# Kernel tuning notes

Hardware: AMD Instinct MI355X
Metric: run time of the kernel (lower is better)

The kernel has to match this reference:

```python
import jax, jax.numpy as jnp
import numpy as np

N = 100000        # num nodes
E = 3_200_000     # num edges
NFEAT, NHID, NCLASS = 256, 128, 40
BN_EPS = 1e-5


def _gcn_norm(edge_index, edge_weight, num_nodes):
    """PyG gcn_norm with self-loops (fill value 1.0): returns (src, dst, norm)."""
    loop = jnp.arange(num_nodes)
    src = jnp.concatenate([edge_index[0], loop])
    dst = jnp.concatenate([edge_index[1], loop])
    ew = jnp.concatenate([edge_weight, jnp.ones((num_nodes,), edge_weight.dtype)])
    deg = jax.ops.segment_sum(ew, dst, num_segments=num_nodes)
    dinv = jnp.where(deg > 0, jax.lax.rsqrt(jnp.maximum(deg, 1e-30)), 0.0)
    norm = dinv[src] * ew * dinv[dst]  # [E+N]
    return src, dst, norm


def _gcn_layer(h, W, b, src, dst, norm, num_nodes):
    lin = h @ W                                   # [N, out]
    msg = lin[src] * norm[:, None]                # gather + scale  [E+N, out]
    agg = jax.ops.segment_sum(msg, dst, num_segments=num_nodes)
    return agg + b


def _bn(h, gamma, beta):
    # BatchNorm1d in training mode: biased batch statistics
    m = jnp.mean(h, axis=0)
    v = jnp.mean(jnp.square(h - m), axis=0)
    return (h - m) * jax.lax.rsqrt(v + BN_EPS) * gamma + beta


def setup_inputs() -> dict:
    key = jax.random.key(0)
    ks = jax.random.split(key, 12)
    s_in = 1.0 / np.sqrt(NFEAT)
    s_h = 1.0 / np.sqrt(NHID)
    return {
        "x": jax.random.normal(ks[0], (N, NFEAT), jnp.float32),
        "edge_index": jax.random.randint(ks[1], (2, E), 0, N, dtype=jnp.int32),
        "edge_weight": jax.random.uniform(ks[2], (E,), jnp.float32),
        "W1": jax.random.normal(ks[3], (NFEAT, NHID), jnp.float32) * s_in,
        "b1": jnp.zeros((NHID,), jnp.float32),
        "g1": jnp.ones((NHID,), jnp.float32),
        "beta1": jnp.zeros((NHID,), jnp.float32),
        "W2": jax.random.normal(ks[4], (NHID, NHID), jnp.float32) * s_h,
        "b2": jnp.zeros((NHID,), jnp.float32),
        "g2": jnp.ones((NHID,), jnp.float32),
        "beta2": jnp.zeros((NHID,), jnp.float32),
        "W3": jax.random.normal(ks[5], (NHID, NHID), jnp.float32) * s_h,
        "b3": jnp.zeros((NHID,), jnp.float32),
        "g3": jnp.ones((NHID,), jnp.float32),
        "beta3": jnp.zeros((NHID,), jnp.float32),
        "linW": jax.random.normal(ks[6], (3 * NHID, NCLASS), jnp.float32) / np.sqrt(3 * NHID),
        "linb": jnp.zeros((NCLASS,), jnp.float32),
    }


def reference(x, edge_index, edge_weight,
              W1, b1, g1, beta1,
              W2, b2, g2, beta2,
              W3, b3, g3, beta3,
              linW, linb):
    src, dst, norm = _gcn_norm(edge_index, edge_weight, N)
    x1 = _bn(jax.nn.relu(_gcn_layer(x, W1, b1, src, dst, norm, N)), g1, beta1)
    x2 = _bn(jax.nn.relu(_gcn_layer(x1, W2, b2, src, dst, norm, N)), g2, beta2)
    x3 = _bn(_gcn_layer(x2, W3, b3, src, dst, norm, N), g3, beta3)  # note: no relu on x3
    embed_x = jnp.concatenate([x1, x2, x3], axis=1)  # [N, 3*NHID]
    logits = embed_x @ linW + linb                   # [N, NCLASS]
    return logits, jax.nn.softmax(logits, axis=1), embed_x
```

## Files before the change

### kernel.cpp

```cpp
#include <hip/hip_runtime.h>
#include <hip/hip_bf16.h>
#include <hip/hip_fp16.h>
#include <math.h>

#define NN 100000
#define NE 3200000
#define NF 256
#define NH 128
#define NC 40
#define BN_EPS 1e-5f

typedef __attribute__((ext_vector_type(8))) short bf16x8;
typedef __attribute__((ext_vector_type(4))) float f32x4;

__device__ __forceinline__ float2 bf2_unpack(unsigned int v) {
    return make_float2(__uint_as_float(v << 16), __uint_as_float(v & 0xffff0000u));
}
__device__ __forceinline__ unsigned int pack2bf(float lo, float hi) {
    unsigned int a = (unsigned int)__hip_bfloat16_raw(__float2bfloat16(lo)).x;
    unsigned int b = (unsigned int)__hip_bfloat16_raw(__float2bfloat16(hi)).x;
    return a | (b << 16);
}

__global__ __launch_bounds__(256) void k_init(unsigned long long* hist, float* sums) {
    int i = blockIdx.x * 256 + threadIdx.x;
    if (i < NN) hist[i] = 0ULL;
    if (i < 3 * 1024) sums[i] = 0.0f;
}

__global__ __launch_bounds__(256) void k_edge(const int* __restrict__ ei, const float* __restrict__ ew,
                                              unsigned long long* __restrict__ hist,
                                              int* __restrict__ pos) {
    int e = blockIdx.x * 256 + threadIdx.x;
    if (e >= NE) return;
    int d = __builtin_nontemporal_load(&ei[NE + e]);
    float w = __builtin_nontemporal_load(&ew[e]);
    unsigned long long pack = (1ULL << 44) | (unsigned long long)(w * 4294967296.0f);
    unsigned long long old = atomicAdd(&hist[d], pack);
    __builtin_nontemporal_store((int)(old >> 44), &pos[e]);
}

__global__ __launch_bounds__(256) void k_dinv(const unsigned long long* __restrict__ hist,
                                              float* __restrict__ dinv) {
    int i = blockIdx.x * 256 + threadIdx.x;
    if (i < NN) {
        float ws = (float)(hist[i] & 0xFFFFFFFFFFFULL) * 2.3283064365386963e-10f;
        dinv[i] = rsqrtf(1.0f + ws);
    }
}

__global__ __launch_bounds__(1024) void k_scan(const unsigned long long* __restrict__ hist,
                                               int* __restrict__ rowptr) {
    __shared__ int wsum[16];
    __shared__ int s_carry;
    int t = threadIdx.x;
    int lane = t & 63, wid = t >> 6;
    if (t == 0) s_carry = 0;
    __syncthreads();
    for (int base = 0; base < NN; base += 4096) {
        int i0 = base + t * 4;
        int c[4];
#pragma unroll
        for (int j = 0; j < 4; j++) {
            int i = i0 + j;
            c[j] = (i < NN) ? (int)(hist[i] >> 44) : 0;
        }
        int v = c[0] + c[1] + c[2] + c[3];
        int x = v;
#pragma unroll
        for (int off = 1; off < 64; off <<= 1) {
            int y = __shfl_up(x, off);
            if (lane >= off) x += y;
        }
        if (lane == 63) wsum[wid] = x;
        __syncthreads();
        if (wid == 0 && lane < 16) {
            int s = wsum[lane];
#pragma unroll
            for (int off = 1; off < 16; off <<= 1) {
                int y = __shfl_up(s, off);
                if (lane >= off) s += y;
            }
            wsum[lane] = s;
        }
        __syncthreads();
        int woff = (wid > 0) ? wsum[wid - 1] : 0;
        int incl = x + woff;
        int carry = s_carry;
        int run = carry + incl - v;
#pragma unroll
        for (int j = 0; j < 4; j++) {
            int i = i0 + j;
            if (i < NN) rowptr[i] = run;
            run += c[j];
        }
        __syncthreads();
        if (t == 1023) s_carry = carry + incl;
        __syncthreads();
    }
    if (t == 0) rowptr[NN] = s_carry;
}

__global__ __launch_bounds__(256) void k_scatter(const int* __restrict__ ei, const float* __restrict__ ew,
                                                 const float* __restrict__ dinv,
                                                 const int* __restrict__ rowptr,
                                                 const int* __restrict__ pos,
                                                 unsigned int* __restrict__ cw) {
    int e = blockIdx.x * 256 + threadIdx.x;
    if (e >= NE) return;
    int s = __builtin_nontemporal_load(&ei[e]);
    int d = __builtin_nontemporal_load(&ei[NE + e]);
    float w = __builtin_nontemporal_load(&ew[e]);
    float nv = dinv[s] * w * dinv[d];
    unsigned int h = (unsigned int)__half_as_ushort(__float2half(nv)) & 0x7fffu;
    unsigned int packed = (unsigned int)s | (h << 17);
    int p = __builtin_nontemporal_load(&pos[e]);
    __builtin_nontemporal_store(packed, &cw[rowptr[d] + p]);
}

template <int K>
__global__ __launch_bounds__(256) void k_gemm_mfma(const float* __restrict__ H, int ldh,
                                                   const float* __restrict__ W,
                                                   __hip_bfloat16* __restrict__ out) {
    __shared__ unsigned int Bt[128][20];
    int t = threadIdx.x;
    int wid = t >> 6, l = t & 63;
    int l15 = l & 15, lhi = l >> 4;
    int rowbase = blockIdx.x * 128 + wid * 32;

    int ar0 = rowbase + l15;      if (ar0 >= NN) ar0 = NN - 1;
    int ar1 = rowbase + 16 + l15; if (ar1 >= NN) ar1 = NN - 1;

    f32x4 acc[2][8];
#pragma unroll
    for (int rt = 0; rt < 2; rt++)
#pragma unroll
        for (int ct = 0; ct < 8; ct++) acc[rt][ct] = (f32x4){0.f, 0.f, 0.f, 0.f};

    for (int kb = 0; kb < K / 32; kb++) {
        __syncthreads();
        for (int i = t; i < 2048; i += 256) {
            int c = i & 127, k2l = i >> 7;
            int k = kb * 32 + 2 * k2l;
            Bt[c][k2l] = pack2bf(W[(size_t)k * NH + c], W[(size_t)(k + 1) * NH + c]);
        }
        __syncthreads();
        const float4* a0p = (const float4*)&H[(size_t)ar0 * ldh + kb * 32 + lhi * 8];
        const float4* a1p = (const float4*)&H[(size_t)ar1 * ldh + kb * 32 + lhi * 8];
        float4 x0 = a0p[0], x1 = a0p[1];
        float4 y0 = a1p[0], y1 = a1p[1];
        union { unsigned int u[4]; bf16x8 v; } af0, af1;
        af0.u[0] = pack2bf(x0.x, x0.y); af0.u[1] = pack2bf(x0.z, x0.w);
        af0.u[2] = pack2bf(x1.x, x1.y); af0.u[3] = pack2bf(x1.z, x1.w);
        af1.u[0] = pack2bf(y0.x, y0.y); af1.u[1] = pack2bf(y0.z, y0.w);
        af1.u[2] = pack2bf(y1.x, y1.y); af1.u[3] = pack2bf(y1.z, y1.w);
#pragma unroll
        for (int ct = 0; ct < 8; ct++) {
            bf16x8 b = *(const bf16x8*)&Bt[ct * 16 + l15][lhi * 4];
            acc[0][ct] = __builtin_amdgcn_mfma_f32_16x16x32_bf16(af0.v, b, acc[0][ct], 0, 0, 0);
            acc[1][ct] = __builtin_amdgcn_mfma_f32_16x16x32_bf16(af1.v, b, acc[1][ct], 0, 0, 0);
        }
    }
#pragma unroll
    for (int rt = 0; rt < 2; rt++)
#pragma unroll
        for (int ct = 0; ct < 8; ct++)
#pragma unroll
            for (int reg = 0; reg < 4; reg++) {
                int row = rowbase + rt * 16 + lhi * 4 + reg;
                if (row < NN)
                    out[(size_t)row * NH + ct * 16 + l15] = __float2bfloat16(acc[rt][ct][reg]);
            }
}

__global__ __launch_bounds__(256) void k_agg(const unsigned int* __restrict__ linb,
                                             const float* __restrict__ dinv,
                                             const int* __restrict__ rowptr,
                                             const unsigned int* __restrict__ cw,
                                             const float* __restrict__ bias,
                                             float* __restrict__ outp, int do_relu) {
    int t = threadIdx.x;
    int node = blockIdx.x * 4 + (t >> 6);
    if (node >= NN) return;
    int ch = t & 63;
    int c = ch << 1;
    float di = dinv[node];
    float2 sv = bf2_unpack(linb[(size_t)node * 64 + ch]);
    float a0 = fmaf(sv.x, di * di, bias[c]);
    float a1 = fmaf(sv.y, di * di, bias[c + 1]);
    int beg = rowptr[node], end = rowptr[node + 1];
    int j = beg;
    for (; j + 16 <= end; j += 16) {
        unsigned int pk[16];
#pragma unroll
        for (int q = 0; q < 16; q++) pk[q] = cw[j + q];
        unsigned int v[16];
#pragma unroll
        for (int q = 0; q < 16; q++) v[q] = linb[(size_t)(pk[q] & 0x1FFFFu) * 64 + ch];
#pragma unroll
        for (int q = 0; q < 16; q++) {
            float w = __half2float(__ushort_as_half((unsigned short)(pk[q] >> 17)));
            float2 f = bf2_unpack(v[q]);
            a0 = fmaf(f.x, w, a0);
            a1 = fmaf(f.y, w, a1);
        }
    }
    for (; j + 4 <= end; j += 4) {
        unsigned int pk[4];
#pragma unroll
        for (int q = 0; q < 4; q++) pk[q] = cw[j + q];
        unsigned int v[4];
#pragma unroll
        for (int q = 0; q < 4; q++) v[q] = linb[(size_t)(pk[q] & 0x1FFFFu) * 64 + ch];
#pragma unroll
        for (int q = 0; q < 4; q++) {
            float w = __half2float(__ushort_as_half((unsigned short)(pk[q] >> 17)));
            float2 f = bf2_unpack(v[q]);
            a0 = fmaf(f.x, w, a0);
            a1 = fmaf(f.y, w, a1);
        }
    }
    for (; j < end; j++) {
        unsigned int pk = cw[j];
        unsigned int vv = linb[(size_t)(pk & 0x1FFFFu) * 64 + ch];
        float w = __half2float(__ushort_as_half((unsigned short)(pk >> 17)));
        float2 f = bf2_unpack(vv);
        a0 = fmaf(f.x, w, a0);
        a1 = fmaf(f.y, w, a1);
    }
    if (do_relu) { a0 = fmaxf(a0, 0.f); a1 = fmaxf(a1, 0.f); }
    *(float2*)&outp[(size_t)node * 384 + c] = make_float2(a0, a1);
}

__global__ __launch_bounds__(256) void k_stats(const float* __restrict__ pre, float* __restrict__ sums) {
    int t = threadIdx.x;
    int c = t & 127, h = t >> 7;
    float s = 0.f, s2 = 0.f;
    for (int r = blockIdx.x * 2 + h; r < NN; r += gridDim.x * 2) {
        float v = pre[(size_t)r * 384 + c];
        s += v;
        s2 = fmaf(v, v, s2);
    }
    __shared__ float ls[256], ls2[256];
    ls[t] = s; ls2[t] = s2;
    __syncthreads();
    if (t < 128) {
        atomicAdd(&sums[c], ls[t] + ls[t + 128]);
        atomicAdd(&sums[NH + c], ls2[t] + ls2[t + 128]);
    }
}

__global__ void k_bnfinal(float* __restrict__ sums, const float* __restrict__ g,
                          const float* __restrict__ beta) {
    int c = threadIdx.x;
    if (c < NH) {
        float m = sums[c] * (1.0f / NN);
        float v = sums[NH + c] * (1.0f / NN) - m * m;
        float rstd = rsqrtf(v + BN_EPS);
        float sc = g[c] * rstd;
        sums[256 + c] = sc;
        sums[384 + c] = beta[c] - m * sc;
    }
}

__global__ __launch_bounds__(256) void k_bnapply(float* __restrict__ pre, const float* __restrict__ sums) {
    int idx = blockIdx.x * 256 + threadIdx.x;
    if (idx >= NN * 32) return;
    int n = idx >> 5, cp = (idx & 31) << 2;
    float4 sc = *(const float4*)&sums[256 + cp];
    float4 sh = *(const float4*)&sums[384 + cp];
    float4 v = *(float4*)&pre[(size_t)n * 384 + cp];
    v.x = fmaf(v.x, sc.x, sh.x);
    v.y = fmaf(v.y, sc.y, sh.y);
    v.z = fmaf(v.z, sc.z, sh.z);
    v.w = fmaf(v.w, sc.w, sh.w);
    *(float4*)&pre[(size_t)n * 384 + cp] = v;
}

__global__ __launch_bounds__(256) void k_final(const float* __restrict__ embed,
                                               const float* __restrict__ linW,
                                               const float* __restrict__ linb,
                                               float* __restrict__ logits, float* __restrict__ probs) {
    __shared__ unsigned int Wt[3 * 16 * 196];
    int t = threadIdx.x;
    for (int i = t; i < 3 * 16 * 192; i += 256) {
        int ct = i / (16 * 192);
        int rem = i - ct * (16 * 192);
        int c = rem / 192, k2 = rem - c * 192;
        int col = ct * 16 + c;
        float lo = (col < NC) ? linW[(size_t)(2 * k2) * NC + col] : 0.f;
        float hi = (col < NC) ? linW[(size_t)(2 * k2 + 1) * NC + col] : 0.f;
        Wt[(ct * 16 + c) * 196 + k2] = pack2bf(lo, hi);
    }
    __syncthreads();

    int wid = t >> 6, l = t & 63;
    int rowbase = blockIdx.x * 64 + wid * 16;
    int l15 = l & 15, lhi = l >> 4;

    int arow = rowbase + l15;
    if (arow > NN - 1) arow = NN - 1;
    const float4* ap = (const float4*)&embed[(size_t)arow * 384 + lhi * 8];

    f32x4 acc0 = {0.f, 0.f, 0.f, 0.f};
    f32x4 acc1 = {0.f, 0.f, 0.f, 0.f};
    f32x4 acc2 = {0.f, 0.f, 0.f, 0.f};

    for (int kb = 0; kb < 12; kb++) {
        float4 a0 = ap[kb * 8];
        float4 a1 = ap[kb * 8 + 1];
        union { unsigned int u[4]; bf16x8 v; } af;
        af.u[0] = pack2bf(a0.x, a0.y);
        af.u[1] = pack2bf(a0.z, a0.w);
        af.u[2] = pack2bf(a1.x, a1.y);
        af.u[3] = pack2bf(a1.z, a1.w);
        int wbase = kb * 16 + lhi * 4;
        bf16x8 b0 = *(const bf16x8*)&Wt[(0 * 16 + l15) * 196 + wbase];
        bf16x8 b1 = *(const bf16x8*)&Wt[(1 * 16 + l15) * 196 + wbase];
        bf16x8 b2 = *(const bf16x8*)&Wt[(2 * 16 + l15) * 196 + wbase];
        acc0 = __builtin_amdgcn_mfma_f32_16x16x32_bf16(af.v, b0, acc0, 0, 0, 0);
        acc1 = __builtin_amdgcn_mfma_f32_16x16x32_bf16(af.v, b1, acc1, 0, 0, 0);
        acc2 = __builtin_amdgcn_mfma_f32_16x16x32_bf16(af.v, b2, acc2, 0, 0, 0);
    }

    int col0 = 0 * 16 + l15, col1 = 1 * 16 + l15, col2 = 2 * 16 + l15;
    float lb0 = (col0 < NC) ? linb[col0] : 0.f;
    float lb1 = (col1 < NC) ? linb[col1] : 0.f;
    float lb2 = (col2 < NC) ? linb[col2] : 0.f;

#pragma unroll
    for (int reg = 0; reg < 4; reg++) {
        int row = rowbase + lhi * 4 + reg;
        float v0 = acc0[reg] + lb0;
        float v1 = acc1[reg] + lb1;
        float v2 = acc2[reg] + lb2;
        float m = fmaxf(v0, v1);
        if (col2 < NC) m = fmaxf(m, v2);
#pragma unroll
        for (int off = 1; off < 16; off <<= 1) m = fmaxf(m, __shfl_xor(m, off));
        float e0 = __expf(v0 - m);
        float e1 = __expf(v1 - m);
        float e2 = (col2 < NC) ? __expf(v2 - m) : 0.f;
        float s = e0 + e1 + e2;
#pragma unroll
        for (int off = 1; off < 16; off <<= 1) s += __shfl_xor(s, off);
        float inv = 1.0f / s;
        if (row < NN) {
            size_t base = (size_t)row * NC;
            logits[base + col0] = v0;
            probs[base + col0] = e0 * inv;
            logits[base + col1] = v1;
            probs[base + col1] = e1 * inv;
            if (col2 < NC) {
                logits[base + col2] = v2;
                probs[base + col2] = e2 * inv;
            }
        }
    }
}

extern "C" void kernel_launch(void* const* d_in, const int* in_sizes, int n_in,
                              void* d_out, int out_size, void* d_ws, size_t ws_size,
                              hipStream_t stream) {
    const float* x    = (const float*)d_in[0];
    const int*   ei   = (const int*)d_in[1];
    const float* ew   = (const float*)d_in[2];
    const float* W1   = (const float*)d_in[3];
    const float* b1   = (const float*)d_in[4];
    const float* g1   = (const float*)d_in[5];
    const float* be1  = (const float*)d_in[6];
    const float* W2   = (const float*)d_in[7];
    const float* b2   = (const float*)d_in[8];
    const float* g2   = (const float*)d_in[9];
    const float* be2  = (const float*)d_in[10];
    const float* W3   = (const float*)d_in[11];
    const float* b3   = (const float*)d_in[12];
    const float* g3   = (const float*)d_in[13];
    const float* be3  = (const float*)d_in[14];
    const float* linW = (const float*)d_in[15];
    const float* linb = (const float*)d_in[16];

    float* out    = (float*)d_out;
    float* logits = out;
    float* probs  = out + (size_t)NN * NC;
    float* embed  = out + (size_t)2 * NN * NC;

    char* ws = (char*)d_ws;
    size_t off = 0;
    auto alloc = [&](size_t bytes) -> char* {
        char* p = ws + off;
        off = (off + bytes + 255) & ~(size_t)255;
        return p;
    };
    float*              dinv   = (float*)alloc((size_t)NN * 4);
    unsigned long long* hist   = (unsigned long long*)alloc((size_t)NN * 8);
    int*                rowptr = (int*)alloc((size_t)(NN + 1) * 4);
    unsigned int*       cw     = (unsigned int*)alloc((size_t)NE * 4);
    __hip_bfloat16*     lin    = (__hip_bfloat16*)alloc((size_t)NN * NH * 2);
    float*              sums   = (float*)alloc(3 * 1024 * 4);
    int*                pos    = (int*)lin;
    (void)ws_size; (void)in_sizes; (void)n_in; (void)out_size;

    int gN = (NN + 255) / 256;
    int gE = (NE + 255) / 256;
    int gM = (NN + 127) / 128;
    int gA = (NN + 3) / 4;
    int gB = (NN * 32 + 255) / 256;
    int gF = (NN + 63) / 64;

    k_init<<<gN, 256, 0, stream>>>(hist, sums);
    k_edge<<<gE, 256, 0, stream>>>(ei, ew, hist, pos);
    k_dinv<<<gN, 256, 0, stream>>>(hist, dinv);
    k_scan<<<1, 1024, 0, stream>>>(hist, rowptr);
    k_scatter<<<gE, 256, 0, stream>>>(ei, ew, dinv, rowptr, pos, cw);

    k_gemm_mfma<NF><<<gM, 256, 0, stream>>>(x, NF, W1, lin);
    k_agg<<<gA, 256, 0, stream>>>((const unsigned int*)lin, dinv, rowptr, cw, b1, embed + 0, 1);
    k_stats<<<1024, 256, 0, stream>>>(embed + 0, sums + 0);
    k_bnfinal<<<1, 128, 0, stream>>>(sums + 0, g1, be1);
    k_bnapply<<<gB, 256, 0, stream>>>(embed + 0, sums + 0);
    k_gemm_mfma<NH><<<gM, 256, 0, stream>>>(embed + 0, 384, W2, lin);
    k_agg<<<gA, 256, 0, stream>>>((const unsigned int*)lin, dinv, rowptr, cw, b2, embed + 128, 1);
    k_stats<<<1024, 256, 0, stream>>>(embed + 128, sums + 1024);
    k_bnfinal<<<1, 128, 0, stream>>>(sums + 1024, g2, be2);
    k_bnapply<<<gB, 256, 0, stream>>>(embed + 128, sums + 1024);
    k_gemm_mfma<NH><<<gM, 256, 0, stream>>>(embed + 128, 384, W3, lin);
    k_agg<<<gA, 256, 0, stream>>>((const unsigned int*)lin, dinv, rowptr, cw, b3, embed + 256, 0);
    k_stats<<<1024, 256, 0, stream>>>(embed + 256, sums + 2048);
    k_bnfinal<<<1, 128, 0, stream>>>(sums + 2048, g3, be3);
    k_bnapply<<<gB, 256, 0, stream>>>(embed + 256, sums + 2048);
    k_final<<<gF, 256, 0, stream>>>(embed, linW, linb, logits, probs);
}
```

Measured before the change: 1.030 ms.

## Privatize degree histogram into eight copies to cut atomic contention

```diff
diff --git a/kernel.cpp b/kernel.cpp
--- a/kernel.cpp
+++ b/kernel.cpp
@@ -9,6 +9,7 @@
 #define NH 128
 #define NC 40
 #define BN_EPS 1e-5f
+#define NCOPY 8
 
 typedef __attribute__((ext_vector_type(8))) short bf16x8;
 typedef __attribute__((ext_vector_type(4))) float f32x4;
@@ -22,34 +23,48 @@
     return a | (b << 16);
 }
 
-__global__ __launch_bounds__(256) void k_init(unsigned long long* hist, float* sums) {
+__global__ __launch_bounds__(256) void k_init(unsigned long long* hist8, float* sums) {
     int i = blockIdx.x * 256 + threadIdx.x;
-    if (i < NN) hist[i] = 0ULL;
+    if (i < NCOPY * NN) hist8[i] = 0ULL;
     if (i < 3 * 1024) sums[i] = 0.0f;
 }
 
 __global__ __launch_bounds__(256) void k_edge(const int* __restrict__ ei, const float* __restrict__ ew,
-                                              unsigned long long* __restrict__ hist,
+                                              unsigned long long* __restrict__ hist8,
                                               int* __restrict__ pos) {
     int e = blockIdx.x * 256 + threadIdx.x;
     if (e >= NE) return;
+    int c = blockIdx.x & (NCOPY - 1);
     int d = __builtin_nontemporal_load(&ei[NE + e]);
     float w = __builtin_nontemporal_load(&ew[e]);
     unsigned long long pack = (1ULL << 44) | (unsigned long long)(w * 4294967296.0f);
-    unsigned long long old = atomicAdd(&hist[d], pack);
+    unsigned long long old = atomicAdd(&hist8[(size_t)c * NN + d], pack);
     __builtin_nontemporal_store((int)(old >> 44), &pos[e]);
 }
 
-__global__ __launch_bounds__(256) void k_dinv(const unsigned long long* __restrict__ hist,
-                                              float* __restrict__ dinv) {
+__global__ __launch_bounds__(256) void k_combine(unsigned long long* __restrict__ hist8,
+                                                 float* __restrict__ dinv,
+                                                 int* __restrict__ counts) {
     int i = blockIdx.x * 256 + threadIdx.x;
-    if (i < NN) {
-        float ws = (float)(hist[i] & 0xFFFFFFFFFFFULL) * 2.3283064365386963e-10f;
-        dinv[i] = rsqrtf(1.0f + ws);
-    }
-}
-
-__global__ __launch_bounds__(1024) void k_scan(const unsigned long long* __restrict__ hist,
+    if (i >= NN) return;
+    int tot = 0;
+    unsigned long long wsum = 0;
+    int start[NCOPY];
+#pragma unroll
+    for (int c = 0; c < NCOPY; c++) {
+        unsigned long long h = hist8[(size_t)c * NN + i];
+        start[c] = tot;
+        tot += (int)(h >> 44);
+        wsum += (h & 0xFFFFFFFFFFFULL);
+    }
+#pragma unroll
+    for (int c = 0; c < NCOPY; c++) hist8[(size_t)c * NN + i] = (unsigned long long)start[c];
+    counts[i] = tot;
+    float ws = (float)wsum * 2.3283064365386963e-10f;
+    dinv[i] = rsqrtf(1.0f + ws);
+}
+
+__global__ __launch_bounds__(1024) void k_scan(const int* __restrict__ counts,
                                                int* __restrict__ rowptr) {
     __shared__ int wsum[16];
     __shared__ int s_carry;
@@ -63,7 +78,7 @@
 #pragma unroll
         for (int j = 0; j < 4; j++) {
             int i = i0 + j;
-            c[j] = (i < NN) ? (int)(hist[i] >> 44) : 0;
+            c[j] = (i < NN) ? counts[i] : 0;
         }
         int v = c[0] + c[1] + c[2] + c[3];
         int x = v;
@@ -104,10 +119,12 @@
 __global__ __launch_bounds__(256) void k_scatter(const int* __restrict__ ei, const float* __restrict__ ew,
                                                  const float* __restrict__ dinv,
                                                  const int* __restrict__ rowptr,
+                                                 const unsigned long long* __restrict__ hist8,
                                                  const int* __restrict__ pos,
                                                  unsigned int* __restrict__ cw) {
     int e = blockIdx.x * 256 + threadIdx.x;
     if (e >= NE) return;
+    int c = blockIdx.x & (NCOPY - 1);
     int s = __builtin_nontemporal_load(&ei[e]);
     int d = __builtin_nontemporal_load(&ei[NE + e]);
     float w = __builtin_nontemporal_load(&ew[e]);
@@ -115,7 +132,8 @@
     unsigned int h = (unsigned int)__half_as_ushort(__float2half(nv)) & 0x7fffu;
     unsigned int packed = (unsigned int)s | (h << 17);
     int p = __builtin_nontemporal_load(&pos[e]);
-    __builtin_nontemporal_store(packed, &cw[rowptr[d] + p]);
+    int slot = rowptr[d] + (int)hist8[(size_t)c * NN + d] + p;
+    __builtin_nontemporal_store(packed, &cw[slot]);
 }
 
 template <int K>
@@ -393,7 +411,8 @@
         return p;
     };
     float*              dinv   = (float*)alloc((size_t)NN * 4);
-    unsigned long long* hist   = (unsigned long long*)alloc((size_t)NN * 8);
+    unsigned long long* hist8  = (unsigned long long*)alloc((size_t)NCOPY * NN * 8);
+    int*                counts = (int*)alloc((size_t)NN * 4);
     int*                rowptr = (int*)alloc((size_t)(NN + 1) * 4);
     unsigned int*       cw     = (unsigned int*)alloc((size_t)NE * 4);
     __hip_bfloat16*     lin    = (__hip_bfloat16*)alloc((size_t)NN * NH * 2);
@@ -402,17 +421,18 @@
     (void)ws_size; (void)in_sizes; (void)n_in; (void)out_size;
 
     int gN = (NN + 255) / 256;
+    int g8 = (NCOPY * NN + 255) / 256;
     int gE = (NE + 255) / 256;
     int gM = (NN + 127) / 128;
     int gA = (NN + 3) / 4;
     int gB = (NN * 32 + 255) / 256;
     int gF = (NN + 63) / 64;
 
-    k_init<<<gN, 256, 0, stream>>>(hist, sums);
-    k_edge<<<gE, 256, 0, stream>>>(ei, ew, hist, pos);
-    k_dinv<<<gN, 256, 0, stream>>>(hist, dinv);
-    k_scan<<<1, 1024, 0, stream>>>(hist, rowptr);
-    k_scatter<<<gE, 256, 0, stream>>>(ei, ew, dinv, rowptr, pos, cw);
+    k_init<<<g8, 256, 0, stream>>>(hist8, sums);
+    k_edge<<<gE, 256, 0, stream>>>(ei, ew, hist8, pos);
+    k_combine<<<gN, 256, 0, stream>>>(hist8, dinv, counts);
+    k_scan<<<1, 1024, 0, stream>>>(counts, rowptr);
+    k_scatter<<<gE, 256, 0, stream>>>(ei, ew, dinv, rowptr, hist8, pos, cw);
 
     k_gemm_mfma<NF><<<gM, 256, 0, stream>>>(x, NF, W1, lin);
     k_agg<<<gA, 256, 0, stream>>>((const unsigned int*)lin, dinv, rowptr, cw, b1, embed + 0, 1);
```

Measured after the change: 1.039 ms. About the same (+0.9%).

## Fuse BN apply into following GEMMs and co-launch layer-1 GEMM with edge histogram

Applied to the files above, without the earlier changes.

```diff
diff --git a/kernel.cpp b/kernel.cpp
--- a/kernel.cpp
+++ b/kernel.cpp
@@ -21,6 +21,13 @@
     unsigned int b = (unsigned int)__hip_bfloat16_raw(__float2bfloat16(hi)).x;
     return a | (b << 16);
 }
+__device__ __forceinline__ float4 affine4(float4 v, float4 sc, float4 sh) {
+    v.x = fmaf(v.x, sc.x, sh.x);
+    v.y = fmaf(v.y, sc.y, sh.y);
+    v.z = fmaf(v.z, sc.z, sh.z);
+    v.w = fmaf(v.w, sc.w, sh.w);
+    return v;
+}
 
 __global__ __launch_bounds__(256) void k_init(unsigned long long* hist, float* sums) {
     int i = blockIdx.x * 256 + threadIdx.x;
@@ -28,16 +35,99 @@
     if (i < 3 * 1024) sums[i] = 0.0f;
 }
 
-__global__ __launch_bounds__(256) void k_edge(const int* __restrict__ ei, const float* __restrict__ ew,
-                                              unsigned long long* __restrict__ hist,
-                                              int* __restrict__ pos) {
-    int e = blockIdx.x * 256 + threadIdx.x;
-    if (e >= NE) return;
-    int d = __builtin_nontemporal_load(&ei[NE + e]);
-    float w = __builtin_nontemporal_load(&ew[e]);
-    unsigned long long pack = (1ULL << 44) | (unsigned long long)(w * 4294967296.0f);
-    unsigned long long old = atomicAdd(&hist[d], pack);
-    __builtin_nontemporal_store((int)(old >> 44), &pos[e]);
+template <int K, bool BN>
+__device__ __forceinline__ void gemm_body(unsigned int (*Bt)[20], const float* H, float* Hw,
+                                          const float* scsh, int ldh, const float* W,
+                                          __hip_bfloat16* out, int blk, int t) {
+    int wid = t >> 6, l = t & 63;
+    int l15 = l & 15, lhi = l >> 4;
+    int rowbase = blk * 128 + wid * 32;
+    int ar0 = rowbase + l15;      if (ar0 >= NN) ar0 = NN - 1;
+    int ar1 = rowbase + 16 + l15; if (ar1 >= NN) ar1 = NN - 1;
+
+    f32x4 acc[2][8];
+#pragma unroll
+    for (int rt = 0; rt < 2; rt++)
+#pragma unroll
+        for (int ct = 0; ct < 8; ct++) acc[rt][ct] = (f32x4){0.f, 0.f, 0.f, 0.f};
+
+    for (int kb = 0; kb < K / 32; kb++) {
+        __syncthreads();
+        for (int i = t; i < 2048; i += 256) {
+            int c = i & 127, k2l = i >> 7;
+            int k = kb * 32 + 2 * k2l;
+            Bt[c][k2l] = pack2bf(W[(size_t)k * NH + c], W[(size_t)(k + 1) * NH + c]);
+        }
+        __syncthreads();
+        int kk = kb * 32 + lhi * 8;
+        const float4* a0p = (const float4*)&H[(size_t)ar0 * ldh + kk];
+        const float4* a1p = (const float4*)&H[(size_t)ar1 * ldh + kk];
+        float4 x0 = a0p[0], x1 = a0p[1];
+        float4 y0 = a1p[0], y1 = a1p[1];
+        if constexpr (BN) {
+            float4 sc0 = *(const float4*)&scsh[kk];
+            float4 sc1 = *(const float4*)&scsh[kk + 4];
+            float4 sh0 = *(const float4*)&scsh[128 + kk];
+            float4 sh1 = *(const float4*)&scsh[128 + kk + 4];
+            x0 = affine4(x0, sc0, sh0); x1 = affine4(x1, sc1, sh1);
+            y0 = affine4(y0, sc0, sh0); y1 = affine4(y1, sc1, sh1);
+            *(float4*)&Hw[(size_t)ar0 * ldh + kk] = x0;
+            *(float4*)&Hw[(size_t)ar0 * ldh + kk + 4] = x1;
+            *(float4*)&Hw[(size_t)ar1 * ldh + kk] = y0;
+            *(float4*)&Hw[(size_t)ar1 * ldh + kk + 4] = y1;
+        }
+        union { unsigned int u[4]; bf16x8 v; } af0, af1;
+        af0.u[0] = pack2bf(x0.x, x0.y); af0.u[1] = pack2bf(x0.z, x0.w);
+        af0.u[2] = pack2bf(x1.x, x1.y); af0.u[3] = pack2bf(x1.z, x1.w);
+        af1.u[0] = pack2bf(y0.x, y0.y); af1.u[1] = pack2bf(y0.z, y0.w);
+        af1.u[2] = pack2bf(y1.x, y1.y); af1.u[3] = pack2bf(y1.z, y1.w);
+#pragma unroll
+        for (int ct = 0; ct < 8; ct++) {
+            bf16x8 b = *(const bf16x8*)&Bt[ct * 16 + l15][lhi * 4];
+            acc[0][ct] = __builtin_amdgcn_mfma_f32_16x16x32_bf16(af0.v, b, acc[0][ct], 0, 0, 0);
+            acc[1][ct] = __builtin_amdgcn_mfma_f32_16x16x32_bf16(af1.v, b, acc[1][ct], 0, 0, 0);
+        }
+    }
+#pragma unroll
+    for (int rt = 0; rt < 2; rt++)
+#pragma unroll
+        for (int ct = 0; ct < 8; ct++)
+#pragma unroll
+            for (int reg = 0; reg < 4; reg++) {
+                int row = rowbase + rt * 16 + lhi * 4 + reg;
+                if (row < NN)
+                    out[(size_t)row * NH + ct * 16 + l15] = __float2bfloat16(acc[rt][ct][reg]);
+            }
+}
+
+__global__ __launch_bounds__(256) void k_g1edge(const float* __restrict__ x, const float* __restrict__ W1,
+                                                __hip_bfloat16* __restrict__ lin,
+                                                const int* __restrict__ ei, const float* __restrict__ ew,
+                                                unsigned long long* __restrict__ hist,
+                                                int* __restrict__ pos, int gm) {
+    __shared__ unsigned int Bt[128][20];
+    int t = threadIdx.x;
+    int blk = (int)blockIdx.x;
+    if (blk < gm) {
+        gemm_body<NF, false>(Bt, x, nullptr, nullptr, NF, W1, lin, blk, t);
+    } else {
+        int e = (blk - gm) * 256 + t;
+        if (e < NE) {
+            int d = __builtin_nontemporal_load(&ei[NE + e]);
+            float w = __builtin_nontemporal_load(&ew[e]);
+            unsigned long long pk = (1ULL << 44) | (unsigned long long)(w * 4294967296.0f);
+            unsigned long long old = atomicAdd(&hist[d], pk);
+            __builtin_nontemporal_store((int)(old >> 44), &pos[e]);
+        }
+    }
+}
+
+__global__ __launch_bounds__(256) void k_gemm_bn(const float* H, float* Hw,
+                                                 const float* __restrict__ scsh,
+                                                 const float* __restrict__ W,
+                                                 __hip_bfloat16* __restrict__ out) {
+    __shared__ unsigned int Bt[128][20];
+    gemm_body<NH, true>(Bt, H, Hw, scsh, 384, W, out, (int)blockIdx.x, (int)threadIdx.x);
 }
 
 __global__ __launch_bounds__(256) void k_dinv(const unsigned long long* __restrict__ hist,
@@ -116,61 +206,6 @@
     unsigned int packed = (unsigned int)s | (h << 17);
     int p = __builtin_nontemporal_load(&pos[e]);
     __builtin_nontemporal_store(packed, &cw[rowptr[d] + p]);
-}
-
-template <int K>
-__global__ __launch_bounds__(256) void k_gemm_mfma(const float* __restrict__ H, int ldh,
-                                                   const float* __restrict__ W,
-                                                   __hip_bfloat16* __restrict__ out) {
-    __shared__ unsigned int Bt[128][20];
-    int t = threadIdx.x;
-    int wid = t >> 6, l = t & 63;
-    int l15 = l & 15, lhi = l >> 4;
-    int rowbase = blockIdx.x * 128 + wid * 32;
-
-    int ar0 = rowbase + l15;      if (ar0 >= NN) ar0 = NN - 1;
-    int ar1 = rowbase + 16 + l15; if (ar1 >= NN) ar1 = NN - 1;
-
-    f32x4 acc[2][8];
-#pragma unroll
-    for (int rt = 0; rt < 2; rt++)
-#pragma unroll
-        for (int ct = 0; ct < 8; ct++) acc[rt][ct] = (f32x4){0.f, 0.f, 0.f, 0.f};
-
-    for (int kb = 0; kb < K / 32; kb++) {
-        __syncthreads();
-        for (int i = t; i < 2048; i += 256) {
-            int c = i & 127, k2l = i >> 7;
-            int k = kb * 32 + 2 * k2l;
-            Bt[c][k2l] = pack2bf(W[(size_t)k * NH + c], W[(size_t)(k + 1) * NH + c]);
-        }
-        __syncthreads();
-        const float4* a0p = (const float4*)&H[(size_t)ar0 * ldh + kb * 32 + lhi * 8];
-        const float4* a1p = (const float4*)&H[(size_t)ar1 * ldh + kb * 32 + lhi * 8];
-        float4 x0 = a0p[0], x1 = a0p[1];
-        float4 y0 = a1p[0], y1 = a1p[1];
-        union { unsigned int u[4]; bf16x8 v; } af0, af1;
-        af0.u[0] = pack2bf(x0.x, x0.y); af0.u[1] = pack2bf(x0.z, x0.w);
-        af0.u[2] = pack2bf(x1.x, x1.y); af0.u[3] = pack2bf(x1.z, x1.w);
-        af1.u[0] = pack2bf(y0.x, y0.y); af1.u[1] = pack2bf(y0.z, y0.w);
-        af1.u[2] = pack2bf(y1.x, y1.y); af1.u[3] = pack2bf(y1.z, y1.w);
-#pragma unroll
-        for (int ct = 0; ct < 8; ct++) {
-            bf16x8 b = *(const bf16x8*)&Bt[ct * 16 + l15][lhi * 4];
-            acc[0][ct] = __builtin_amdgcn_mfma_f32_16x16x32_bf16(af0.v, b, acc[0][ct], 0, 0, 0);
-            acc[1][ct] = __builtin_amdgcn_mfma_f32_16x16x32_bf16(af1.v, b, acc[1][ct], 0, 0, 0);
-        }
-    }
-#pragma unroll
-    for (int rt = 0; rt < 2; rt++)
-#pragma unroll
-        for (int ct = 0; ct < 8; ct++)
-#pragma unroll
-            for (int reg = 0; reg < 4; reg++) {
-                int row = rowbase + rt * 16 + lhi * 4 + reg;
-                if (row < NN)
-                    out[(size_t)row * NH + ct * 16 + l15] = __float2bfloat16(acc[rt][ct][reg]);
-            }
 }
 
 __global__ __launch_bounds__(256) void k_agg(const unsigned int* __restrict__ linb,
@@ -263,21 +298,8 @@
     }
 }
 
-__global__ __launch_bounds__(256) void k_bnapply(float* __restrict__ pre, const float* __restrict__ sums) {
-    int idx = blockIdx.x * 256 + threadIdx.x;
-    if (idx >= NN * 32) return;
-    int n = idx >> 5, cp = (idx & 31) << 2;
-    float4 sc = *(const float4*)&sums[256 + cp];
-    float4 sh = *(const float4*)&sums[384 + cp];
-    float4 v = *(float4*)&pre[(size_t)n * 384 + cp];
-    v.x = fmaf(v.x, sc.x, sh.x);
-    v.y = fmaf(v.y, sc.y, sh.y);
-    v.z = fmaf(v.z, sc.z, sh.z);
-    v.w = fmaf(v.w, sc.w, sh.w);
-    *(float4*)&pre[(size_t)n * 384 + cp] = v;
-}
-
-__global__ __launch_bounds__(256) void k_final(const float* __restrict__ embed,
+__global__ __launch_bounds__(256) void k_final(const float* __restrict__ embed, float* embedW,
+                                               const float* __restrict__ scsh3,
                                                const float* __restrict__ linW,
                                                const float* __restrict__ linb,
                                                float* __restrict__ logits, float* __restrict__ probs) {
@@ -309,6 +331,17 @@
     for (int kb = 0; kb < 12; kb++) {
         float4 a0 = ap[kb * 8];
         float4 a1 = ap[kb * 8 + 1];
+        if (kb >= 8) {
+            int kk = kb * 32 + lhi * 8 - 256;
+            float4 sc0 = *(const float4*)&scsh3[kk];
+            float4 sc1 = *(const float4*)&scsh3[kk + 4];
+            float4 sh0 = *(const float4*)&scsh3[128 + kk];
+            float4 sh1 = *(const float4*)&scsh3[128 + kk + 4];
+            a0 = affine4(a0, sc0, sh0);
+            a1 = affine4(a1, sc1, sh1);
+            *(float4*)&embedW[(size_t)arow * 384 + kb * 32 + lhi * 8] = a0;
+            *(float4*)&embedW[(size_t)arow * 384 + kb * 32 + lhi * 8 + 4] = a1;
+        }
         union { unsigned int u[4]; bf16x8 v; } af;
         af.u[0] = pack2bf(a0.x, a0.y);
         af.u[1] = pack2bf(a0.z, a0.w);
@@ -397,37 +430,32 @@
     int*                rowptr = (int*)alloc((size_t)(NN + 1) * 4);
     unsigned int*       cw     = (unsigned int*)alloc((size_t)NE * 4);
     __hip_bfloat16*     lin    = (__hip_bfloat16*)alloc((size_t)NN * NH * 2);
+    int*                pos    = (int*)alloc((size_t)NE * 4);
     float*              sums   = (float*)alloc(3 * 1024 * 4);
-    int*                pos    = (int*)lin;
     (void)ws_size; (void)in_sizes; (void)n_in; (void)out_size;
 
     int gN = (NN + 255) / 256;
     int gE = (NE + 255) / 256;
     int gM = (NN + 127) / 128;
     int gA = (NN + 3) / 4;
-    int gB = (NN * 32 + 255) / 256;
     int gF = (NN + 63) / 64;
 
     k_init<<<gN, 256, 0, stream>>>(hist, sums);
-    k_edge<<<gE, 256, 0, stream>>>(ei, ew, hist, pos);
+    k_g1edge<<<gM + gE, 256, 0, stream>>>(x, W1, lin, ei, ew, hist, pos, gM);
     k_dinv<<<gN, 256, 0, stream>>>(hist, dinv);
     k_scan<<<1, 1024, 0, stream>>>(hist, rowptr);
     k_scatter<<<gE, 256, 0, stream>>>(ei, ew, dinv, rowptr, pos, cw);
 
-    k_gemm_mfma<NF><<<gM, 256, 0, stream>>>(x, NF, W1, lin);
     k_agg<<<gA, 256, 0, stream>>>((const unsigned int*)lin, dinv, rowptr, cw, b1, embed + 0, 1);
     k_stats<<<1024, 256, 0, stream>>>(embed + 0, sums + 0);
     k_bnfinal<<<1, 128, 0, stream>>>(sums + 0, g1, be1);
-    k_bnapply<<<gB, 256, 0, stream>>>(embed + 0, sums + 0);
-    k_gemm_mfma<NH><<<gM, 256, 0, stream>>>(embed + 0, 384, W2, lin);
+    k_gemm_bn<<<gM, 256, 0, stream>>>(embed + 0, embed + 0, sums + 256, W2, lin);
     k_agg<<<gA, 256, 0, stream>>>((const unsigned int*)lin, dinv, rowptr, cw, b2, embed + 128, 1);
     k_stats<<<1024, 256, 0, stream>>>(embed + 128, sums + 1024);
     k_bnfinal<<<1, 128, 0, stream>>>(sums + 1024, g2, be2);
-    k_bnapply<<<gB, 256, 0, stream>>>(embed + 128, sums + 1024);
-    k_gemm_mfma<NH><<<gM, 256, 0, stream>>>(embed + 128, 384, W3, lin);
+    k_gemm_bn<<<gM, 256, 0, stream>>>(embed + 128, embed + 128, sums + 1024 + 256, W3, lin);
     k_agg<<<gA, 256, 0, stream>>>((const unsigned int*)lin, dinv, rowptr, cw, b3, embed + 256, 0);
     k_stats<<<1024, 256, 0, stream>>>(embed + 256, sums + 2048);
     k_bnfinal<<<1, 128, 0, stream>>>(sums + 2048, g3, be3);
-    k_bnapply<<<gB, 256, 0, stream>>>(embed + 256, sums + 2048);
-    k_final<<<gF, 256, 0, stream>>>(embed, linW, linb, logits, probs);
-}
+    k_final<<<gF, 256, 0, stream>>>(embed, embed, sums + 2048 + 256, linW, linb, logits, probs);
+}
```

Result: faster. 989.6 us (-3.9%).
